# Kernel optimization log

Measured on AMD Instinct MI355X. Metric: run time of the kernel, lower is better.

## Reference

```python
import jax, jax.numpy as jnp
import numpy as np

B, F_IN, N_D, N_A, VBS, N_STEPS = 1024, 256, 64, 64, 128, 3
FO = N_D + N_A            # 128
D_CAT = 2 * F_IN          # 512
AD = F_IN                 # attention_dim = 256
GAMMA, EPSILON, BN_EPS = 1.3, 1e-15, 1e-5
SQRT_HALF = 0.7071067811865476


def _bn(x, w, b):
    # full-batch BatchNorm1d (training mode, biased var)
    m = x.mean(0)
    v = x.var(0)
    return (x - m) / jnp.sqrt(v + BN_EPS) * w + b


def _gbn(x, w, b):
    # Ghost BatchNorm: per virtual-batch statistics
    n, f = x.shape
    xr = x.reshape(n // VBS, VBS, f)
    m = xr.mean(1, keepdims=True)
    v = xr.var(1, keepdims=True)
    return (xr - m).reshape(n, f) / jnp.sqrt(v + BN_EPS).repeat(VBS, axis=0).reshape(n, f) * w + b


def _glu(x, fcw, bnw, bnb):
    h = _gbn(x @ fcw.T, bnw, bnb)
    d = h.shape[-1] // 2
    return h[:, :d] * jax.nn.sigmoid(h[:, d:])


def _feat_transformer(x, fc0, bnw0, bnb0, fc1, bnw1, bnb1):
    # independent GLU block, first=True, n_glu_independent=2
    h = _glu(x, fc0, bnw0, bnb0)
    return (h + _glu(h, fc1, bnw1, bnb1)) * SQRT_HALF


def _sparsemax(z):
    f = z.shape[-1]
    zs = -jnp.sort(-z, axis=-1)                      # descending
    k = jnp.arange(1, f + 1, dtype=z.dtype)
    zc = jnp.cumsum(zs, axis=-1)
    support = (1.0 + k * zs) > zc
    kz = jnp.sum(support, axis=-1, keepdims=True)
    tau = (jnp.take_along_axis(zc, kz - 1, axis=-1) - 1.0) / kz.astype(z.dtype)
    return jnp.maximum(z - tau, 0.0)


def _self_attn_1d(x, in_w, in_b, out_w, out_b):
    # nn.MultiheadAttention(embed_dim=1, heads=1) over the feature axis
    q = x * in_w[0] + in_b[0]
    k = x * in_w[1] + in_b[1]
    v = x * in_w[2] + in_b[2]
    attn = jax.nn.softmax(jnp.einsum('bi,bj->bij', q, k), axis=-1)  # scale 1/sqrt(1)
    y = jnp.einsum('bij,bj->bi', attn, v) * out_w + out_b
    return y, attn


def setup_inputs() -> dict:
    key = jax.random.key(0)
    ks = iter(jax.random.split(key, 32))
    s = 0.1
    d = {
        'x': jax.random.normal(next(ks), (B, F_IN), jnp.float32),
        'bemv': jax.random.normal(next(ks), (B, F_IN), jnp.float32),
        'gmat': jax.random.uniform(next(ks), (AD, F_IN), jnp.float32),
        'bn_w': jnp.ones((F_IN,), jnp.float32),
        'bn_b': jnp.zeros((F_IN,), jnp.float32),
        'init_fc0': jax.random.normal(next(ks), (2 * FO, D_CAT), jnp.float32) * s,
        'init_bnw0': jnp.ones((2 * FO,), jnp.float32),
        'init_bnb0': jnp.zeros((2 * FO,), jnp.float32),
        'init_fc1': jax.random.normal(next(ks), (2 * FO, FO), jnp.float32) * s,
        'init_bnw1': jnp.ones((2 * FO,), jnp.float32),
        'init_bnb1': jnp.zeros((2 * FO,), jnp.float32),
        'step_fc0': jax.random.normal(next(ks), (N_STEPS, 2 * FO, D_CAT), jnp.float32) * s,
        'step_bnw0': jnp.ones((N_STEPS, 2 * FO), jnp.float32),
        'step_bnb0': jnp.zeros((N_STEPS, 2 * FO), jnp.float32),
        'step_fc1': jax.random.normal(next(ks), (N_STEPS, 2 * FO, FO), jnp.float32) * s,
        'step_bnw1': jnp.ones((N_STEPS, 2 * FO), jnp.float32),
        'step_bnb1': jnp.zeros((N_STEPS, 2 * FO), jnp.float32),
        'att_fc': jax.random.normal(next(ks), (N_STEPS, AD, N_A), jnp.float32) * s,
        'att_bnw': jnp.ones((N_STEPS, AD), jnp.float32),
        'att_bnb': jnp.zeros((N_STEPS, AD), jnp.float32),
        'sa_in_w': jax.random.normal(next(ks), (N_STEPS, 3), jnp.float32),
        'sa_in_b': jnp.zeros((N_STEPS, 3), jnp.float32),
        'sa_out_w': jax.random.normal(next(ks), (N_STEPS,), jnp.float32),
        'sa_out_b': jnp.zeros((N_STEPS,), jnp.float32),
    }
    return d


def reference(x, bemv, gmat, bn_w, bn_b,
              init_fc0, init_bnw0, init_bnb0, init_fc1, init_bnw1, init_bnb1,
              step_fc0, step_bnw0, step_bnb0, step_fc1, step_bnw1, step_bnb1,
              att_fc, att_bnw, att_bnb,
              sa_in_w, sa_in_b, sa_out_w, sa_out_b):
    prior = jnp.ones((x.shape[0], AD), x.dtype)
    xn = _bn(x, bn_w, bn_b)
    x_cat = jnp.concatenate([xn, bemv], axis=1)
    feat_out = _feat_transformer(x_cat, init_fc0, init_bnw0, init_bnb0,
                                 init_fc1, init_bnw1, init_bnb1)
    att = feat_out[:, N_D:]
    m_loss = jnp.asarray(0.0, x.dtype)
    steps, amaps = [], []
    for s in range(N_STEPS):
        a = _gbn(att @ att_fc[s].T, att_bnw[s], att_bnb[s])
        tab_mask = _sparsemax(a * prior)
        m_loss = m_loss + jnp.mean(jnp.sum(tab_mask * jnp.log(tab_mask + EPSILON), axis=1))
        prior = prior * (GAMMA - tab_mask)
        x_masked = (tab_mask @ gmat) * xn
        x_masked, A = _self_attn_1d(x_masked, sa_in_w[s], sa_in_b[s], sa_out_w[s], sa_out_b[s])
        amaps.append(A)
        feat_out = _feat_transformer(jnp.concatenate([x_masked, bemv], axis=1),
                                     step_fc0[s], step_bnw0[s], step_bnb0[s],
                                     step_fc1[s], step_bnw1[s], step_bnb1[s])
        steps.append(jax.nn.leaky_relu(feat_out[:, :N_D], 0.01))
        att = feat_out[:, N_D:]
    m_loss = m_loss / N_STEPS
    return jnp.stack(steps), m_loss, jnp.stack(amaps)
```

## Files before the change

### kernel.cpp

```cpp
#include <hip/hip_runtime.h>
#include <hip/hip_bf16.h>

#define BATCH 1024
#define F_IN 256
#define N_D 64
#define N_A 64
#define VBS 128
#define N_STEPS 3
#define FO 128
#define D_CAT 512
#define AD 256
#define GAMMA_C 1.3f
#define BN_EPS_C 1e-5f
#define SQRT_HALF_C 0.70710678118654752440f

__device__ __forceinline__ float ldin(const void* p, size_t i, int isbf){
  if (isbf) return __bfloat162float(((const __hip_bfloat16*)p)[i]);
  return ((const float*)p)[i];
}
__device__ __forceinline__ float4 ld4(const void* p, size_t i, int isbf){
  if (!isbf) return *(const float4*)((const float*)p + i);
  const __hip_bfloat16* q = (const __hip_bfloat16*)p + i;
  return make_float4(__bfloat162float(q[0]), __bfloat162float(q[1]),
                     __bfloat162float(q[2]), __bfloat162float(q[3]));
}

__device__ __forceinline__ float wsum(float v){
#pragma unroll
  for (int o = 32; o > 0; o >>= 1) v += __shfl_xor(v, o);
  return v;
}
__device__ __forceinline__ float wmaxr(float v){
#pragma unroll
  for (int o = 32; o > 0; o >>= 1) v = fmaxf(v, __shfl_xor(v, o));
  return v;
}
__device__ __forceinline__ float wminr(float v){
#pragma unroll
  for (int o = 32; o > 0; o >>= 1) v = fminf(v, __shfl_xor(v, o));
  return v;
}
__device__ __forceinline__ float block_sum(float v, float* sb){
  int t = threadIdx.x;
  sb[t] = v; __syncthreads();
#pragma unroll
  for (int s = 128; s > 0; s >>= 1){
    if (t < s) sb[t] += sb[t + s];
    __syncthreads();
  }
  float r = sb[0]; __syncthreads();
  return r;
}

__global__ void detect_k(const unsigned short* __restrict__ u, float* __restrict__ flag){
  __shared__ int cnt;
  if (threadIdx.x == 0) cnt = 0;
  __syncthreads();
  int c = 0;
  for (int j = 0; j < 16; ++j){
    unsigned short v = u[(size_t)(threadIdx.x * 16 + j) * 2];
    int e = (v >> 7) & 0xFF;
    if (e >= 118 && e <= 134) c++;
  }
  atomicAdd(&cnt, c);
  __syncthreads();
  if (threadIdx.x == 0) flag[0] = (cnt > 2048) ? 1.0f : 0.0f;
}

__global__ void bnstats_k(const void* __restrict__ x, float* __restrict__ mean,
                          float* __restrict__ istd, const float* __restrict__ flg){
  __shared__ float sb[256];
  const int isbf = flg[0] != 0.0f;
  int f = blockIdx.x, t = threadIdx.x;
  float s = 0.f, ss = 0.f;
  for (int r = t; r < BATCH; r += 256){
    float v = ldin(x, (size_t)r * F_IN + f, isbf);
    s += v; ss += v * v;
  }
  s  = block_sum(s, sb);
  ss = block_sum(ss, sb);
  if (t == 0){
    float m = s * (1.f / BATCH);
    mean[f] = m;
    istd[f] = rsqrtf(ss * (1.f / BATCH) - m * m + BN_EPS_C);
  }
}

__global__ void xn_k(const void* __restrict__ x, const float* __restrict__ mean,
                     const float* __restrict__ istd, const void* __restrict__ bw,
                     const void* __restrict__ bb, float* __restrict__ xn,
                     const float* __restrict__ flg){
  const int isbf = flg[0] != 0.0f;
  int idx = blockIdx.x * 256 + threadIdx.x;
  int f = idx & (F_IN - 1);
  xn[idx] = (ldin(x, idx, isbf) - mean[f]) * istd[f] * ldin(bw, f, isbf) + ldin(bb, f, isbf);
}

__global__ __launch_bounds__(256)
void gemm_bt_k(const float* __restrict__ A1, const void* __restrict__ A2, int split,
               const void* __restrict__ W, size_t woff, float* __restrict__ C,
               int K, const float* __restrict__ flg){
  __shared__ float As[32][34];
  __shared__ float Ws[32][34];
  const int isbf = flg[0] != 0.0f;
  const int n0 = blockIdx.x * 32, m0 = blockIdx.y * 32;
  const int t = threadIdx.x;
  const int tx = t & 15, ty = t >> 4;
  const int lr = t >> 3, lk = (t & 7) * 4;
  const int nc = K >> 5;
  float a00 = 0.f, a01 = 0.f, a10 = 0.f, a11 = 0.f;

  auto lda = [&](int k0) -> float4 {
    int gk = k0 + lk, gr = m0 + lr;
    if (gk < split) return *(const float4*)(A1 + (size_t)gr * split + gk);
    return ld4(A2, (size_t)gr * (K - split) + (gk - split), isbf);
  };
  auto ldw = [&](int k0) -> float4 {
    return ld4(W, woff + (size_t)(n0 + lr) * K + k0 + lk, isbf);
  };

  float4 ra = lda(0), rw = ldw(0);
  for (int c = 0; c < nc; ++c){
    As[lk+0][lr] = ra.x; As[lk+1][lr] = ra.y; As[lk+2][lr] = ra.z; As[lk+3][lr] = ra.w;
    Ws[lk+0][lr] = rw.x; Ws[lk+1][lr] = rw.y; Ws[lk+2][lr] = rw.z; Ws[lk+3][lr] = rw.w;
    __syncthreads();
    float4 na = ra, nw = rw;
    if (c + 1 < nc){ na = lda((c+1) << 5); nw = ldw((c+1) << 5); }
#pragma unroll
    for (int kk = 0; kk < 32; ++kk){
      float2 av = *(const float2*)&As[kk][ty*2];
      float2 wv = *(const float2*)&Ws[kk][tx*2];
      a00 += av.x * wv.x; a01 += av.x * wv.y;
      a10 += av.y * wv.x; a11 += av.y * wv.y;
    }
    __syncthreads();
    ra = na; rw = nw;
  }
  int r0 = m0 + ty*2, c0 = n0 + tx*2;
  float* Cp = C + (size_t)r0 * 256 + c0;
  Cp[0] = a00; Cp[1] = a01; Cp[256] = a10; Cp[257] = a11;
}

__global__ __launch_bounds__(256)
void gstats_k(const float* __restrict__ H, const void* __restrict__ w,
              const void* __restrict__ b, size_t off, float* __restrict__ sa,
              float* __restrict__ sb, const float* __restrict__ flg){
  __shared__ float ps[8][32], pss[8][32];
  const int isbf = flg[0] != 0.0f;
  int c0 = blockIdx.x * 32, g = blockIdx.y;
  int tx = threadIdx.x & 31, q = threadIdx.x >> 5;
  const float* Hp = H + ((size_t)g*128 + q*16) * 256 + c0 + tx;
  float s = 0.f, ss = 0.f;
#pragma unroll
  for (int i = 0; i < 16; ++i){ float v = Hp[(size_t)i*256]; s += v; ss += v*v; }
  ps[q][tx] = s; pss[q][tx] = ss;
  __syncthreads();
  if (threadIdx.x < 32){
    int t = threadIdx.x, col = c0 + t;
    float S = 0.f, SS = 0.f;
#pragma unroll
    for (int qq = 0; qq < 8; ++qq){ S += ps[qq][t]; SS += pss[qq][t]; }
    float m = S * (1.f/128), is = rsqrtf(SS * (1.f/128) - m*m + BN_EPS_C);
    float wv = ldin(w, off + col, isbf), bv = ldin(b, off + col, isbf);
    float A = is * wv;
    sa[g*256 + col] = A;
    sb[g*256 + col] = bv - m * A;
  }
}

__global__ __launch_bounds__(256)
void spmax_k(const float* __restrict__ H, const float* __restrict__ sa,
             const float* __restrict__ sb, float* __restrict__ prior,
             float* __restrict__ tab, float* __restrict__ lrow, int first){
  int lane = threadIdx.x & 63, wv = threadIdx.x >> 6;
  int b = blockIdx.x * 4 + wv, g = b >> 7;
  size_t rb = (size_t)b * 256;
  float z[4], pr[4];
#pragma unroll
  for (int e = 0; e < 4; ++e){
    int j = e*64 + lane;
    pr[e] = first ? 1.f : prior[rb + j];
    z[e] = (H[rb + j] * sa[g*256 + j] + sb[g*256 + j]) * pr[e];
  }
  float zm = wmaxr(fmaxf(fmaxf(z[0], z[1]), fmaxf(z[2], z[3])));
  float lo = zm - 1.f, hi = zm;
#pragma unroll 1
  for (int it = 0; it < 30; ++it){
    float mid = 0.5f * (lo + hi);
    float s = 0.f;
#pragma unroll
    for (int e = 0; e < 4; ++e){ float d = z[e] - mid; s += d > 0.f ? d : 0.f; }
    s = wsum(s);
    if (s >= 1.f) lo = mid; else hi = mid;
  }
  float tau = 0.5f * (lo + hi);
  float ls = 0.f;
#pragma unroll
  for (int e = 0; e < 4; ++e){
    int j = e*64 + lane;
    float p = z[e] - tau; p = p > 0.f ? p : 0.f;
    tab[rb + j]   = p;
    prior[rb + j] = pr[e] * (GAMMA_C - p);
    ls += p * __logf(p + 1e-15f);
  }
  ls = wsum(ls);
  if (lane == 0) lrow[b] = ls;
}

__global__ __launch_bounds__(256)
void attn_k(const float* __restrict__ tab, const void* __restrict__ gmat,
            const float* __restrict__ xn, float* __restrict__ y,
            const void* __restrict__ in_w, const void* __restrict__ in_b,
            const void* __restrict__ out_w, const void* __restrict__ out_b,
            int s, float* __restrict__ amap, const float* __restrict__ flg){
  __shared__ __align__(16) float tabs[256], qs[256], ks[256], vs[256], ms[256], rz[256];
  __shared__ float r1[4], r2[4];
  const int isbf = flg[0] != 0.0f;
  int b = blockIdx.x, t = threadIdx.x;
  tabs[t] = tab[(size_t)b*256 + t];
  __syncthreads();
  float xm = 0.f;
  if (isbf){
    const __hip_bfloat16* gm = (const __hip_bfloat16*)gmat;
#pragma unroll 8
    for (int k2 = 0; k2 < 256; ++k2) xm += tabs[k2] * __bfloat162float(gm[k2*256 + t]);
  } else {
    const float* gm = (const float*)gmat;
#pragma unroll 8
    for (int k2 = 0; k2 < 256; ++k2) xm += tabs[k2] * gm[k2*256 + t];
  }
  xm *= xn[(size_t)b*256 + t];
  float w0 = ldin(in_w, s*3+0, isbf), w1 = ldin(in_w, s*3+1, isbf), w2 = ldin(in_w, s*3+2, isbf);
  float b0 = ldin(in_b, s*3+0, isbf), b1 = ldin(in_b, s*3+1, isbf), b2 = ldin(in_b, s*3+2, isbf);
  float ow = ldin(out_w, s, isbf), ob = ldin(out_b, s, isbf);
  float q = xm*w0 + b0, k = xm*w1 + b1, v = xm*w2 + b2;
  qs[t] = q; ks[t] = k; vs[t] = v;
  int lane = t & 63, wv = t >> 6;
  float km = wmaxr(k), kn = wminr(k);
  if (lane == 0){ r1[wv] = km; r2[wv] = kn; }
  __syncthreads();
  float kmax = fmaxf(fmaxf(r1[0], r1[1]), fmaxf(r1[2], r1[3]));
  float kmin = fminf(fminf(r2[0], r2[1]), fminf(r2[2], r2[3]));
  float mi = (q >= 0.f) ? q*kmax : q*kmin;
  float Z = 0.f, Y = 0.f;
#pragma unroll 8
  for (int j = 0; j < 256; j += 4){
    float4 k4 = *(const float4*)&ks[j];
    float4 v4 = *(const float4*)&vs[j];
    float e0 = __expf(q*k4.x - mi), e1 = __expf(q*k4.y - mi);
    float e2 = __expf(q*k4.z - mi), e3 = __expf(q*k4.w - mi);
    Z += (e0 + e1) + (e2 + e3);
    Y += (e0*v4.x + e1*v4.y) + (e2*v4.z + e3*v4.w);
  }
  float rzv = 1.f / Z;
  y[(size_t)b*256 + t] = Y*rzv*ow + ob;
  ms[t] = mi; rz[t] = rzv;
  __syncthreads();
  int c0 = (t & 127) * 2;
  int rh = (t >> 7) * 128;
  float k0 = ks[c0], k1 = ks[c0 + 1];
  size_t base = ((size_t)s*BATCH + b) * 65536 + c0;
#pragma unroll 8
  for (int i = 0; i < 128; i += 4){
    int r = rh + i;
    float4 q4 = *(const float4*)&qs[r];
    float4 m4 = *(const float4*)&ms[r];
    float4 s4 = *(const float4*)&rz[r];
    float e00 = __expf(q4.x*k0 - m4.x) * s4.x, e01 = __expf(q4.x*k1 - m4.x) * s4.x;
    float e10 = __expf(q4.y*k0 - m4.y) * s4.y, e11 = __expf(q4.y*k1 - m4.y) * s4.y;
    float e20 = __expf(q4.z*k0 - m4.z) * s4.z, e21 = __expf(q4.z*k1 - m4.z) * s4.z;
    float e30 = __expf(q4.w*k0 - m4.w) * s4.w, e31 = __expf(q4.w*k1 - m4.w) * s4.w;
    *(float2*)(amap + base + (size_t)(r+0)*256) = make_float2(e00, e01);
    *(float2*)(amap + base + (size_t)(r+1)*256) = make_float2(e10, e11);
    *(float2*)(amap + base + (size_t)(r+2)*256) = make_float2(e20, e21);
    *(float2*)(amap + base + (size_t)(r+3)*256) = make_float2(e30, e31);
  }
}

template<int MODE>
__global__ __launch_bounds__(256)
void gbnglu_k(const float* __restrict__ H, const void* __restrict__ w,
              const void* __restrict__ b, size_t off, const float* __restrict__ G0,
              float* __restrict__ Gout, float* __restrict__ att,
              float* __restrict__ steps_out, const float* __restrict__ flg){
  __shared__ float ps[4][64], pss[4][64];
  __shared__ float sA[64], sB[64];
  const int isbf = flg[0] != 0.0f;
  int c0 = blockIdx.x * 32, g = blockIdx.y;
  int t = threadIdx.x;
  int tx = t & 63, q = t >> 6;
  int cc = tx & 31, half = tx >> 5;
  int col = c0 + cc + half*128;
  const float* Hp = H + ((size_t)g*128 + q*32) * 256 + col;
  float s = 0.f, ss = 0.f;
#pragma unroll
  for (int i = 0; i < 32; ++i){ float v = Hp[(size_t)i*256]; s += v; ss += v*v; }
  ps[q][tx] = s; pss[q][tx] = ss;
  __syncthreads();
  if (t < 64){
    float S  = ps[0][t] + ps[1][t] + ps[2][t] + ps[3][t];
    float SS = pss[0][t] + pss[1][t] + pss[2][t] + pss[3][t];
    float m  = S * (1.f/128), is = rsqrtf(SS * (1.f/128) - m*m + BN_EPS_C);
    int colT = c0 + (t & 31) + (t >> 5)*128;
    float wv = ldin(w, off + colT, isbf), bv = ldin(b, off + colT, isbf);
    float A = is * wv;
    sA[t] = A; sB[t] = bv - m*A;
  }
  __syncthreads();
  int oc = t & 31;
  int rbase = (t >> 5) * 16;
#pragma unroll
  for (int i = 0; i < 16; ++i){
    int r = g*128 + rbase + i;
    float h0 = H[(size_t)r*256 + c0 + oc];
    float h1 = H[(size_t)r*256 + c0 + oc + 128];
    float n0 = h0 * sA[oc]    + sB[oc];
    float n1 = h1 * sA[32+oc] + sB[32+oc];
    float gl = n0 / (1.f + __expf(-n1));
    int j = c0 + oc;
    if constexpr (MODE == 0){
      Gout[(size_t)r*128 + j] = gl;
    } else {
      float f = (G0[(size_t)r*128 + j] + gl) * SQRT_HALF_C;
      if (j < 64){
        if (steps_out) steps_out[(size_t)r*64 + j] = f > 0.f ? f : 0.01f*f;
      } else {
        att[(size_t)r*64 + (j - 64)] = f;
      }
    }
  }
}

__global__ void mloss_k(const float* __restrict__ lrow, float* __restrict__ outp){
  __shared__ float sb[256];
  int t = threadIdx.x;
  float s = 0.f;
  for (int i = t; i < N_STEPS*BATCH; i += 256) s += lrow[i];
  s = block_sum(s, sb);
  if (t == 0) outp[0] = s * (1.f/(N_STEPS*(float)BATCH));
}

extern "C" void kernel_launch(void* const* d_in, const int* in_sizes, int n_in,
                              void* d_out, int out_size, void* d_ws, size_t ws_size,
                              hipStream_t stream){
  const void* x         = d_in[0];
  const void* bemv      = d_in[1];
  const void* gmat      = d_in[2];
  const void* bn_w      = d_in[3];
  const void* bn_b      = d_in[4];
  const void* init_fc0  = d_in[5];
  const void* init_bnw0 = d_in[6];
  const void* init_bnb0 = d_in[7];
  const void* init_fc1  = d_in[8];
  const void* init_bnw1 = d_in[9];
  const void* init_bnb1 = d_in[10];
  const void* step_fc0  = d_in[11];
  const void* step_bnw0 = d_in[12];
  const void* step_bnb0 = d_in[13];
  const void* step_fc1  = d_in[14];
  const void* step_bnw1 = d_in[15];
  const void* step_bnb1 = d_in[16];
  const void* att_fc    = d_in[17];
  const void* att_bnw   = d_in[18];
  const void* att_bnb   = d_in[19];
  const void* sa_in_w   = d_in[20];
  const void* sa_in_b   = d_in[21];
  const void* sa_out_w  = d_in[22];
  const void* sa_out_b  = d_in[23];

  float* out       = (float*)d_out;
  float* steps_out = out;
  float* mloss_out = out + (size_t)N_STEPS*BATCH*N_D;
  float* amaps     = mloss_out + 1;

  float* w     = (float*)d_ws;
  float* mean  = w;
  float* istd  = w + 256;
  float* flag  = w + 512;
  float* lrow  = w + 1024;
  float* sa    = w + 4096;
  float* sbuf  = sa + 2048;
  float* xn    = sbuf + 2048;
  float* H     = xn   + 262144;
  float* G0    = H    + 262144;
  float* att   = G0   + 131072;
  float* tab   = att  + 65536;
  float* prior = tab  + 262144;
  float* y     = prior + 262144;

  dim3 gemmGrid(8, 32);
  dim3 gluGrid(4, 8);
  dim3 gstGrid(8, 8);

  detect_k<<<1, 256, 0, stream>>>((const unsigned short*)x, flag);
  bnstats_k<<<256, 256, 0, stream>>>(x, mean, istd, flag);
  xn_k<<<1024, 256, 0, stream>>>(x, mean, istd, bn_w, bn_b, xn, flag);

  gemm_bt_k<<<gemmGrid, 256, 0, stream>>>(xn, bemv, 256, init_fc0, 0, H, 512, flag);
  gbnglu_k<0><<<gluGrid, 256, 0, stream>>>(H, init_bnw0, init_bnb0, 0, nullptr, G0, nullptr, nullptr, flag);
  gemm_bt_k<<<gemmGrid, 256, 0, stream>>>(G0, nullptr, 128, init_fc1, 0, H, 128, flag);
  gbnglu_k<1><<<gluGrid, 256, 0, stream>>>(H, init_bnw1, init_bnb1, 0, G0, nullptr, att, nullptr, flag);

  for (int s = 0; s < N_STEPS; ++s){
    gemm_bt_k<<<gemmGrid, 256, 0, stream>>>(att, nullptr, 64, att_fc, (size_t)s*AD*N_A, H, 64, flag);
    gstats_k<<<gstGrid, 256, 0, stream>>>(H, att_bnw, att_bnb, (size_t)s*256, sa, sbuf, flag);
    spmax_k<<<256, 256, 0, stream>>>(H, sa, sbuf, prior, tab, lrow + s*1024, s == 0);
    attn_k<<<1024, 256, 0, stream>>>(tab, gmat, xn, y, sa_in_w, sa_in_b, sa_out_w, sa_out_b, s, amaps, flag);
    gemm_bt_k<<<gemmGrid, 256, 0, stream>>>(y, bemv, 256, step_fc0, (size_t)s*256*512, H, 512, flag);
    gbnglu_k<0><<<gluGrid, 256, 0, stream>>>(H, step_bnw0, step_bnb0, (size_t)s*256, nullptr, G0, nullptr, nullptr, flag);
    gemm_bt_k<<<gemmGrid, 256, 0, stream>>>(G0, nullptr, 128, step_fc1, (size_t)s*256*128, H, 128, flag);
    gbnglu_k<1><<<gluGrid, 256, 0, stream>>>(H, step_bnw1, step_bnb1, (size_t)s*256, G0, nullptr, att,
                                             steps_out + (size_t)s*BATCH*N_D, flag);
  }
  mloss_k<<<1, 256, 0, stream>>>(lrow, mloss_out);
}
```

Baseline: 448.9 us.

## Fuse GBN-GLU into GEMM loads, fuse sparsemax with sparse gmat product

The GBN+GLU normalisation is now applied while the second GEMM loads its operands, so the materialised G0 buffer goes away, and a separate combine kernel recomputes the first GLU for the residual. Sparsemax is fused with the tab_mask@gmat product. That product uses a per-4-feature ballot mask to skip all-zero chunks of the sparse mask and reuses each gmat load across four rows. The goals are fewer HBM round-trips and much less gmat traffic compared with the per-row dense 256x256 matvec in attn_k. In exchange, the GLU exponentials are recomputed inside the GEMM and there are extra gstats launches.

```diff
diff --git a/kernel.cpp b/kernel.cpp
--- a/kernel.cpp
+++ b/kernel.cpp
@@ -142,6 +142,61 @@
 }
 
 __global__ __launch_bounds__(256)
+void gemm_glu_k(const float* __restrict__ H1, const float* __restrict__ saf,
+                const float* __restrict__ sbf, const void* __restrict__ W,
+                size_t woff, float* __restrict__ C, const float* __restrict__ flg){
+  __shared__ float As[32][34];
+  __shared__ float Ws[32][34];
+  const int isbf = flg[0] != 0.0f;
+  const int n0 = blockIdx.x * 32, m0 = blockIdx.y * 32;
+  const int t = threadIdx.x;
+  const int tx = t & 15, ty = t >> 4;
+  const int lr = t >> 3, lk = (t & 7) * 4;
+  float a00 = 0.f, a01 = 0.f, a10 = 0.f, a11 = 0.f;
+
+  auto lda = [&](int k0) -> float4 {
+    int gk = k0 + lk, gr = m0 + lr, g = gr >> 7;
+    float4 h0 = *(const float4*)(H1 + (size_t)gr*256 + gk);
+    float4 h1 = *(const float4*)(H1 + (size_t)gr*256 + gk + 128);
+    float4 A0 = *(const float4*)(saf + g*256 + gk);
+    float4 B0 = *(const float4*)(sbf + g*256 + gk);
+    float4 A1 = *(const float4*)(saf + g*256 + gk + 128);
+    float4 B1 = *(const float4*)(sbf + g*256 + gk + 128);
+    float4 r;
+    r.x = (h0.x*A0.x + B0.x) / (1.f + __expf(-(h1.x*A1.x + B1.x)));
+    r.y = (h0.y*A0.y + B0.y) / (1.f + __expf(-(h1.y*A1.y + B1.y)));
+    r.z = (h0.z*A0.z + B0.z) / (1.f + __expf(-(h1.z*A1.z + B1.z)));
+    r.w = (h0.w*A0.w + B0.w) / (1.f + __expf(-(h1.w*A1.w + B1.w)));
+    return r;
+  };
+  auto ldw = [&](int k0) -> float4 {
+    return ld4(W, woff + (size_t)(n0 + lr) * 128 + k0 + lk, isbf);
+  };
+
+  float4 ra = lda(0), rw = ldw(0);
+#pragma unroll 1
+  for (int c = 0; c < 4; ++c){
+    As[lk+0][lr] = ra.x; As[lk+1][lr] = ra.y; As[lk+2][lr] = ra.z; As[lk+3][lr] = ra.w;
+    Ws[lk+0][lr] = rw.x; Ws[lk+1][lr] = rw.y; Ws[lk+2][lr] = rw.z; Ws[lk+3][lr] = rw.w;
+    __syncthreads();
+    float4 na = ra, nw = rw;
+    if (c + 1 < 4){ na = lda((c+1) << 5); nw = ldw((c+1) << 5); }
+#pragma unroll
+    for (int kk = 0; kk < 32; ++kk){
+      float2 av = *(const float2*)&As[kk][ty*2];
+      float2 wv = *(const float2*)&Ws[kk][tx*2];
+      a00 += av.x * wv.x; a01 += av.x * wv.y;
+      a10 += av.y * wv.x; a11 += av.y * wv.y;
+    }
+    __syncthreads();
+    ra = na; rw = nw;
+  }
+  int r0 = m0 + ty*2, c0 = n0 + tx*2;
+  float* Cp = C + (size_t)r0 * 256 + c0;
+  Cp[0] = a00; Cp[1] = a01; Cp[256] = a10; Cp[257] = a11;
+}
+
+__global__ __launch_bounds__(256)
 void gstats_k(const float* __restrict__ H, const void* __restrict__ w,
               const void* __restrict__ b, size_t off, float* __restrict__ sa,
               float* __restrict__ sb, const float* __restrict__ flg){
@@ -169,19 +224,30 @@
 }
 
 __global__ __launch_bounds__(256)
-void spmax_k(const float* __restrict__ H, const float* __restrict__ sa,
-             const float* __restrict__ sb, float* __restrict__ prior,
-             float* __restrict__ tab, float* __restrict__ lrow, int first){
+void spmaxxm_k(const float* __restrict__ H, const float* __restrict__ sa,
+               const float* __restrict__ sb, float* __restrict__ prior,
+               const float* __restrict__ xn, const void* __restrict__ gmat,
+               float* __restrict__ xm, float* __restrict__ lrow,
+               int first, const float* __restrict__ flg){
+  __shared__ __align__(16) float tabs[4][256];
+  __shared__ unsigned int msk[4][2];
+  const int isbf = flg[0] != 0.0f;
   int lane = threadIdx.x & 63, wv = threadIdx.x >> 6;
-  int b = blockIdx.x * 4 + wv, g = b >> 7;
+  int b0 = blockIdx.x * 4;
+  int b = b0 + wv, g = b >> 7;
   size_t rb = (size_t)b * 256;
-  float z[4], pr[4];
-#pragma unroll
-  for (int e = 0; e < 4; ++e){
-    int j = e*64 + lane;
-    pr[e] = first ? 1.f : prior[rb + j];
-    z[e] = (H[rb + j] * sa[g*256 + j] + sb[g*256 + j]) * pr[e];
-  }
+  int j0 = lane * 4;
+  float4 h4 = *(const float4*)(H + rb + j0);
+  float4 A4 = *(const float4*)(sa + (size_t)g*256 + j0);
+  float4 B4 = *(const float4*)(sb + (size_t)g*256 + j0);
+  float pr[4];
+  if (first){ pr[0] = pr[1] = pr[2] = pr[3] = 1.f; }
+  else { float4 p4 = *(const float4*)(prior + rb + j0); pr[0]=p4.x; pr[1]=p4.y; pr[2]=p4.z; pr[3]=p4.w; }
+  float z[4];
+  z[0] = (h4.x*A4.x + B4.x) * pr[0];
+  z[1] = (h4.y*A4.y + B4.y) * pr[1];
+  z[2] = (h4.z*A4.z + B4.z) * pr[2];
+  z[3] = (h4.w*A4.w + B4.w) * pr[3];
   float zm = wmaxr(fmaxf(fmaxf(z[0], z[1]), fmaxf(z[2], z[3])));
   float lo = zm - 1.f, hi = zm;
 #pragma unroll 1
@@ -194,46 +260,63 @@
     if (s >= 1.f) lo = mid; else hi = mid;
   }
   float tau = 0.5f * (lo + hi);
-  float ls = 0.f;
+  float p[4], ls = 0.f;
 #pragma unroll
   for (int e = 0; e < 4; ++e){
-    int j = e*64 + lane;
-    float p = z[e] - tau; p = p > 0.f ? p : 0.f;
-    tab[rb + j]   = p;
-    prior[rb + j] = pr[e] * (GAMMA_C - p);
-    ls += p * __logf(p + 1e-15f);
-  }
+    p[e] = z[e] - tau; p[e] = p[e] > 0.f ? p[e] : 0.f;
+    ls += p[e] * __logf(p[e] + 1e-15f);
+  }
+  *(float4*)&tabs[wv][j0] = make_float4(p[0], p[1], p[2], p[3]);
+  *(float4*)(prior + rb + j0) = make_float4(pr[0]*(GAMMA_C - p[0]), pr[1]*(GAMMA_C - p[1]),
+                                            pr[2]*(GAMMA_C - p[2]), pr[3]*(GAMMA_C - p[3]));
   ls = wsum(ls);
   if (lane == 0) lrow[b] = ls;
-}
-
-__global__ __launch_bounds__(256)
-void attn_k(const float* __restrict__ tab, const void* __restrict__ gmat,
-            const float* __restrict__ xn, float* __restrict__ y,
+  bool nz = (p[0] > 0.f) | (p[1] > 0.f) | (p[2] > 0.f) | (p[3] > 0.f);
+  unsigned long long bm = __ballot(nz);
+  if (lane == 0){ msk[wv][0] = (unsigned int)bm; msk[wv][1] = (unsigned int)(bm >> 32); }
+  __syncthreads();
+  int t = threadIdx.x;
+  unsigned long long M0 = msk[0][0] | ((unsigned long long)msk[0][1] << 32);
+  unsigned long long M1 = msk[1][0] | ((unsigned long long)msk[1][1] << 32);
+  unsigned long long M2 = msk[2][0] | ((unsigned long long)msk[2][1] << 32);
+  unsigned long long M3 = msk[3][0] | ((unsigned long long)msk[3][1] << 32);
+  float a0 = 0.f, a1 = 0.f, a2 = 0.f, a3 = 0.f;
+#pragma unroll 1
+  for (int c = 0; c < 64; ++c){
+    int r0a = (int)((M0 >> c) & 1), r1a = (int)((M1 >> c) & 1);
+    int r2a = (int)((M2 >> c) & 1), r3a = (int)((M3 >> c) & 1);
+    if (r0a | r1a | r2a | r3a){
+      int k = c * 4;
+      float g0 = ldin(gmat, (size_t)(k+0)*256 + t, isbf);
+      float g1 = ldin(gmat, (size_t)(k+1)*256 + t, isbf);
+      float g2 = ldin(gmat, (size_t)(k+2)*256 + t, isbf);
+      float g3 = ldin(gmat, (size_t)(k+3)*256 + t, isbf);
+      if (r0a){ float4 tv = *(float4*)&tabs[0][k]; a0 += tv.x*g0 + tv.y*g1 + tv.z*g2 + tv.w*g3; }
+      if (r1a){ float4 tv = *(float4*)&tabs[1][k]; a1 += tv.x*g0 + tv.y*g1 + tv.z*g2 + tv.w*g3; }
+      if (r2a){ float4 tv = *(float4*)&tabs[2][k]; a2 += tv.x*g0 + tv.y*g1 + tv.z*g2 + tv.w*g3; }
+      if (r3a){ float4 tv = *(float4*)&tabs[3][k]; a3 += tv.x*g0 + tv.y*g1 + tv.z*g2 + tv.w*g3; }
+    }
+  }
+  xm[(size_t)(b0+0)*256 + t] = a0 * xn[(size_t)(b0+0)*256 + t];
+  xm[(size_t)(b0+1)*256 + t] = a1 * xn[(size_t)(b0+1)*256 + t];
+  xm[(size_t)(b0+2)*256 + t] = a2 * xn[(size_t)(b0+2)*256 + t];
+  xm[(size_t)(b0+3)*256 + t] = a3 * xn[(size_t)(b0+3)*256 + t];
+}
+
+__global__ __launch_bounds__(256)
+void attn_k(const float* __restrict__ xm, float* __restrict__ y,
             const void* __restrict__ in_w, const void* __restrict__ in_b,
             const void* __restrict__ out_w, const void* __restrict__ out_b,
             int s, float* __restrict__ amap, const float* __restrict__ flg){
-  __shared__ __align__(16) float tabs[256], qs[256], ks[256], vs[256], ms[256], rz[256];
+  __shared__ __align__(16) float qs[256], ks[256], vs[256], ms[256], rz[256];
   __shared__ float r1[4], r2[4];
   const int isbf = flg[0] != 0.0f;
   int b = blockIdx.x, t = threadIdx.x;
-  tabs[t] = tab[(size_t)b*256 + t];
-  __syncthreads();
-  float xm = 0.f;
-  if (isbf){
-    const __hip_bfloat16* gm = (const __hip_bfloat16*)gmat;
-#pragma unroll 8
-    for (int k2 = 0; k2 < 256; ++k2) xm += tabs[k2] * __bfloat162float(gm[k2*256 + t]);
-  } else {
-    const float* gm = (const float*)gmat;
-#pragma unroll 8
-    for (int k2 = 0; k2 < 256; ++k2) xm += tabs[k2] * gm[k2*256 + t];
-  }
-  xm *= xn[(size_t)b*256 + t];
   float w0 = ldin(in_w, s*3+0, isbf), w1 = ldin(in_w, s*3+1, isbf), w2 = ldin(in_w, s*3+2, isbf);
   float b0 = ldin(in_b, s*3+0, isbf), b1 = ldin(in_b, s*3+1, isbf), b2 = ldin(in_b, s*3+2, isbf);
   float ow = ldin(out_w, s, isbf), ob = ldin(out_b, s, isbf);
-  float q = xm*w0 + b0, k = xm*w1 + b1, v = xm*w2 + b2;
+  float xv = xm[(size_t)b*256 + t];
+  float q = xv*w0 + b0, k = xv*w1 + b1, v = xv*w2 + b2;
   qs[t] = q; ks[t] = k; vs[t] = v;
   int lane = t & 63, wv = t >> 6;
   float km = wmaxr(k), kn = wminr(k);
@@ -277,57 +360,27 @@
   }
 }
 
-template<int MODE>
-__global__ __launch_bounds__(256)
-void gbnglu_k(const float* __restrict__ H, const void* __restrict__ w,
-              const void* __restrict__ b, size_t off, const float* __restrict__ G0,
-              float* __restrict__ Gout, float* __restrict__ att,
-              float* __restrict__ steps_out, const float* __restrict__ flg){
-  __shared__ float ps[4][64], pss[4][64];
-  __shared__ float sA[64], sB[64];
-  const int isbf = flg[0] != 0.0f;
-  int c0 = blockIdx.x * 32, g = blockIdx.y;
-  int t = threadIdx.x;
-  int tx = t & 63, q = t >> 6;
-  int cc = tx & 31, half = tx >> 5;
-  int col = c0 + cc + half*128;
-  const float* Hp = H + ((size_t)g*128 + q*32) * 256 + col;
-  float s = 0.f, ss = 0.f;
-#pragma unroll
-  for (int i = 0; i < 32; ++i){ float v = Hp[(size_t)i*256]; s += v; ss += v*v; }
-  ps[q][tx] = s; pss[q][tx] = ss;
-  __syncthreads();
-  if (t < 64){
-    float S  = ps[0][t] + ps[1][t] + ps[2][t] + ps[3][t];
-    float SS = pss[0][t] + pss[1][t] + pss[2][t] + pss[3][t];
-    float m  = S * (1.f/128), is = rsqrtf(SS * (1.f/128) - m*m + BN_EPS_C);
-    int colT = c0 + (t & 31) + (t >> 5)*128;
-    float wv = ldin(w, off + colT, isbf), bv = ldin(b, off + colT, isbf);
-    float A = is * wv;
-    sA[t] = A; sB[t] = bv - m*A;
-  }
-  __syncthreads();
-  int oc = t & 31;
-  int rbase = (t >> 5) * 16;
-#pragma unroll
-  for (int i = 0; i < 16; ++i){
-    int r = g*128 + rbase + i;
-    float h0 = H[(size_t)r*256 + c0 + oc];
-    float h1 = H[(size_t)r*256 + c0 + oc + 128];
-    float n0 = h0 * sA[oc]    + sB[oc];
-    float n1 = h1 * sA[32+oc] + sB[32+oc];
-    float gl = n0 / (1.f + __expf(-n1));
-    int j = c0 + oc;
-    if constexpr (MODE == 0){
-      Gout[(size_t)r*128 + j] = gl;
-    } else {
-      float f = (G0[(size_t)r*128 + j] + gl) * SQRT_HALF_C;
-      if (j < 64){
-        if (steps_out) steps_out[(size_t)r*64 + j] = f > 0.f ? f : 0.01f*f;
-      } else {
-        att[(size_t)r*64 + (j - 64)] = f;
-      }
-    }
+__global__ __launch_bounds__(256)
+void combine_k(const float* __restrict__ H1, const float* __restrict__ sa0,
+               const float* __restrict__ sb0, const float* __restrict__ H2,
+               const float* __restrict__ sa1, const float* __restrict__ sb1,
+               float* __restrict__ att, float* __restrict__ steps_out){
+  int r = blockIdx.x * 2 + (threadIdx.x >> 7);
+  int j = threadIdx.x & 127;
+  int g = r >> 7;
+  float h0 = H1[(size_t)r*256 + j],  h1 = H1[(size_t)r*256 + j + 128];
+  float n0 = h0 * sa0[g*256 + j]     + sb0[g*256 + j];
+  float n1 = h1 * sa0[g*256 + j+128] + sb0[g*256 + j+128];
+  float g0 = n0 / (1.f + __expf(-n1));
+  float h2 = H2[(size_t)r*256 + j],  h3 = H2[(size_t)r*256 + j + 128];
+  float m0 = h2 * sa1[g*256 + j]     + sb1[g*256 + j];
+  float m1 = h3 * sa1[g*256 + j+128] + sb1[g*256 + j+128];
+  float g1 = m0 / (1.f + __expf(-m1));
+  float f = (g0 + g1) * SQRT_HALF_C;
+  if (j < 64){
+    if (steps_out) steps_out[(size_t)r*64 + j] = f > 0.f ? f : 0.01f*f;
+  } else {
+    att[(size_t)r*64 + (j - 64)] = f;
   }
 }
 
@@ -374,43 +427,48 @@
   float* amaps     = mloss_out + 1;
 
   float* w     = (float*)d_ws;
-  float* mean  = w;
-  float* istd  = w + 256;
-  float* flag  = w + 512;
-  float* lrow  = w + 1024;
-  float* sa    = w + 4096;
-  float* sbuf  = sa + 2048;
-  float* xn    = sbuf + 2048;
-  float* H     = xn   + 262144;
-  float* G0    = H    + 262144;
-  float* att   = G0   + 131072;
-  float* tab   = att  + 65536;
-  float* prior = tab  + 262144;
+  float* flag  = w;
+  float* mean  = w + 16;
+  float* istd  = w + 272;
+  float* lrow  = w + 528;
+  float* sa0   = w + 4096;
+  float* sb0   = sa0 + 2048;
+  float* sa1   = sb0 + 2048;
+  float* sb1   = sa1 + 2048;
+  float* saA   = sb1 + 2048;
+  float* sbA   = saA + 2048;
+  float* xn    = w + 16384;
+  float* H1    = xn   + 262144;
+  float* H2    = H1   + 262144;
+  float* att   = H2   + 262144;
+  float* xm    = att  + 65536;
+  float* prior = xm   + 262144;
   float* y     = prior + 262144;
 
   dim3 gemmGrid(8, 32);
-  dim3 gluGrid(4, 8);
   dim3 gstGrid(8, 8);
 
   detect_k<<<1, 256, 0, stream>>>((const unsigned short*)x, flag);
   bnstats_k<<<256, 256, 0, stream>>>(x, mean, istd, flag);
   xn_k<<<1024, 256, 0, stream>>>(x, mean, istd, bn_w, bn_b, xn, flag);
 
-  gemm_bt_k<<<gemmGrid, 256, 0, stream>>>(xn, bemv, 256, init_fc0, 0, H, 512, flag);
-  gbnglu_k<0><<<gluGrid, 256, 0, stream>>>(H, init_bnw0, init_bnb0, 0, nullptr, G0, nullptr, nullptr, flag);
-  gemm_bt_k<<<gemmGrid, 256, 0, stream>>>(G0, nullptr, 128, init_fc1, 0, H, 128, flag);
-  gbnglu_k<1><<<gluGrid, 256, 0, stream>>>(H, init_bnw1, init_bnb1, 0, G0, nullptr, att, nullptr, flag);
+  gemm_bt_k<<<gemmGrid, 256, 0, stream>>>(xn, bemv, 256, init_fc0, 0, H1, 512, flag);
+  gstats_k<<<gstGrid, 256, 0, stream>>>(H1, init_bnw0, init_bnb0, 0, sa0, sb0, flag);
+  gemm_glu_k<<<gemmGrid, 256, 0, stream>>>(H1, sa0, sb0, init_fc1, 0, H2, flag);
+  gstats_k<<<gstGrid, 256, 0, stream>>>(H2, init_bnw1, init_bnb1, 0, sa1, sb1, flag);
+  combine_k<<<512, 256, 0, stream>>>(H1, sa0, sb0, H2, sa1, sb1, att, nullptr);
 
   for (int s = 0; s < N_STEPS; ++s){
-    gemm_bt_k<<<gemmGrid, 256, 0, stream>>>(att, nullptr, 64, att_fc, (size_t)s*AD*N_A, H, 64, flag);
-    gstats_k<<<gstGrid, 256, 0, stream>>>(H, att_bnw, att_bnb, (size_t)s*256, sa, sbuf, flag);
-    spmax_k<<<256, 256, 0, stream>>>(H, sa, sbuf, prior, tab, lrow + s*1024, s == 0);
-    attn_k<<<1024, 256, 0, stream>>>(tab, gmat, xn, y, sa_in_w, sa_in_b, sa_out_w, sa_out_b, s, amaps, flag);
-    gemm_bt_k<<<gemmGrid, 256, 0, stream>>>(y, bemv, 256, step_fc0, (size_t)s*256*512, H, 512, flag);
-    gbnglu_k<0><<<gluGrid, 256, 0, stream>>>(H, step_bnw0, step_bnb0, (size_t)s*256, nullptr, G0, nullptr, nullptr, flag);
-    gemm_bt_k<<<gemmGrid, 256, 0, stream>>>(G0, nullptr, 128, step_fc1, (size_t)s*256*128, H, 128, flag);
-    gbnglu_k<1><<<gluGrid, 256, 0, stream>>>(H, step_bnw1, step_bnb1, (size_t)s*256, G0, nullptr, att,
-                                             steps_out + (size_t)s*BATCH*N_D, flag);
+    gemm_bt_k<<<gemmGrid, 256, 0, stream>>>(att, nullptr, 64, att_fc, (size_t)s*AD*N_A, H1, 64, flag);
+    gstats_k<<<gstGrid, 256, 0, stream>>>(H1, att_bnw, att_bnb, (size_t)s*256, saA, sbA, flag);
+    spmaxxm_k<<<256, 256, 0, stream>>>(H1, saA, sbA, prior, xn, gmat, xm, lrow + s*1024, s == 0, flag);
+    attn_k<<<1024, 256, 0, stream>>>(xm, y, sa_in_w, sa_in_b, sa_out_w, sa_out_b, s, amaps, flag);
+    gemm_bt_k<<<gemmGrid, 256, 0, stream>>>(y, bemv, 256, step_fc0, (size_t)s*256*512, H1, 512, flag);
+    gstats_k<<<gstGrid, 256, 0, stream>>>(H1, step_bnw0, step_bnb0, (size_t)s*256, sa0, sb0, flag);
+    gemm_glu_k<<<gemmGrid, 256, 0, stream>>>(H1, sa0, sb0, step_fc1, (size_t)s*256*128, H2, flag);
+    gstats_k<<<gstGrid, 256, 0, stream>>>(H2, step_bnw1, step_bnb1, (size_t)s*256, sa1, sb1, flag);
+    combine_k<<<512, 256, 0, stream>>>(H1, sa0, sb0, H2, sa1, sb1, att,
+                                       steps_out + (size_t)s*BATCH*N_D);
   }
   mloss_k<<<1, 256, 0, stream>>>(lrow, mloss_out);
 }
```

Measured after the change: 440.4 us. Within noise of the previous version (-1.9%).
